# Optimization experiments

Measured on AMD Instinct MI355X. Metric: run time of the kernel, lower is better.

Reference implementation:

```python
import jax, jax.numpy as jnp
import numpy as np

NUM_HEADS = 12


def setup_inputs() -> dict:
    key = jax.random.key(0)
    ks = jax.random.split(key, 12)
    B, S, H = 8, 1024, 768
    h = jax.random.normal(ks[0], (B, S, H), dtype=jnp.float32)
    att_bias = jax.random.normal(ks[1], (B, S, S, NUM_HEADS), dtype=jnp.float32)
    mask = jax.random.randint(ks[2], (B, S, S), 0, 2, dtype=jnp.int32)
    sc = 1.0 / np.sqrt(H)
    Wq = jax.random.normal(ks[3], (H, H), dtype=jnp.float32) * sc
    bq = jax.random.normal(ks[4], (H,), dtype=jnp.float32) * 0.01
    Wk = jax.random.normal(ks[5], (H, H), dtype=jnp.float32) * sc
    bk = jax.random.normal(ks[6], (H,), dtype=jnp.float32) * 0.01
    Wv = jax.random.normal(ks[7], (H, H), dtype=jnp.float32) * sc
    bv = jax.random.normal(ks[8], (H,), dtype=jnp.float32) * 0.01
    Wo = jax.random.normal(ks[9], (H, H), dtype=jnp.float32) * sc
    bo = jax.random.normal(ks[10], (H,), dtype=jnp.float32) * 0.01
    return {"h": h, "att_bias": att_bias, "mask": mask,
            "Wq": Wq, "bq": bq, "Wk": Wk, "bk": bk,
            "Wv": Wv, "bv": bv, "Wo": Wo, "bo": bo}


def reference(h, att_bias, mask, Wq, bq, Wk, bk, Wv, bv, Wo, bo):
    B, S, H = h.shape
    nh = NUM_HEADS
    d = H // nh
    scale = d ** -0.5
    # projections -> [B, nh, S, d]
    q = (h @ Wq + bq).reshape(B, S, nh, d).transpose(0, 2, 1, 3)
    k = (h @ Wk + bk).reshape(B, S, nh, d).transpose(0, 2, 1, 3)
    v = (h @ Wv + bv).reshape(B, S, nh, d).transpose(0, 2, 1, 3)
    # scores [B, nh, S, S] + additive bias (permuted from [B,S,S,nh])
    scores = jnp.einsum('bhqd,bhkd->bhqk', q, k) * scale
    scores = scores + att_bias.transpose(0, 3, 1, 2)
    # masked_fill with 1e-14 (faithful to original: near-zero score, not -inf)
    scores = jnp.where(mask[:, None, :, :].astype(bool),
                       jnp.asarray(1e-14, scores.dtype), scores)
    attn = jax.nn.softmax(scores, axis=-1)  # dropout p=0 -> identity
    out = jnp.einsum('bhqk,bhkd->bhqd', attn, v)
    out = out.transpose(0, 2, 1, 3).reshape(B, S, H)
    return out @ Wo + bo
```

## Files before the change

kernel.cpp:

```cpp
#include <hip/hip_runtime.h>


typedef __attribute__((ext_vector_type(8))) __bf16 bf16x8;
typedef __attribute__((ext_vector_type(4))) float floatx4;
using bf16 = __bf16;

#define HID 768
#define NHEAD 12
#define DHEAD 64
#define SEQ 1024
#define NBATCH 8
#define WELEM (HID * HID)
#define QKVELEM (NBATCH * NHEAD * SEQ * DHEAD)

__device__ __forceinline__ floatx4 mfma_bf16(bf16x8 a, bf16x8 b, floatx4 c) {
  return __builtin_amdgcn_mfma_f32_16x16x32_bf16(a, b, c, 0, 0, 0);
}

#define ASYNC16(gp, lp)                                           \
  __builtin_amdgcn_global_load_lds(                               \
      (__attribute__((address_space(1))) void*)(gp),              \
      (__attribute__((address_space(3))) void*)(lp), 16, 0, 0)

__global__ void prep_weights(const float* __restrict__ Wq, const float* __restrict__ Wk,
                             const float* __restrict__ Wv, const float* __restrict__ Wo,
                             bf16* __restrict__ WT) {
  __shared__ float t[32][33];
  const int m = blockIdx.z;
  const float* W = (m == 0) ? Wq : (m == 1) ? Wk : (m == 2) ? Wv : Wo;
  const int k0 = blockIdx.x * 32, n0 = blockIdx.y * 32;
  const int tx = threadIdx.x, ty = threadIdx.y;
#pragma unroll
  for (int i = 0; i < 4; ++i)
    t[ty + 8 * i][tx] = W[(size_t)(k0 + ty + 8 * i) * HID + n0 + tx];
  __syncthreads();
  bf16* o = WT + (size_t)m * WELEM;
#pragma unroll
  for (int i = 0; i < 4; ++i)
    o[(size_t)(n0 + ty + 8 * i) * HID + k0 + tx] = (bf16)t[tx][ty + 8 * i];
}

__global__ void prep_h(const float* __restrict__ X, bf16* __restrict__ Y) {
  const size_t i = ((size_t)blockIdx.x * 256 + threadIdx.x) * 8;
  float4 a = *(const float4*)(X + i);
  float4 b = *(const float4*)(X + i + 4);
  bf16x8 o;
  o[0] = (bf16)a.x; o[1] = (bf16)a.y; o[2] = (bf16)a.z; o[3] = (bf16)a.w;
  o[4] = (bf16)b.x; o[5] = (bf16)b.y; o[6] = (bf16)b.z; o[7] = (bf16)b.w;
  *(bf16x8*)(Y + i) = o;
}

__launch_bounds__(256, 2)
__global__ void qkv_gemm(const bf16* __restrict__ A, const bf16* __restrict__ WT,
                         const float* __restrict__ bq, const float* __restrict__ bk,
                         const float* __restrict__ bv,
                         bf16* __restrict__ Qb, bf16* __restrict__ Kb,
                         bf16* __restrict__ Vb) {
  __shared__ __align__(16) bf16 As[128][32];
  __shared__ __align__(16) bf16 Bs[128][32];
  const int mat = blockIdx.z;
  const int bn = blockIdx.x * 128, bm = blockIdx.y * 128;
  const bf16* W = WT + (size_t)mat * WELEM;
  const int tid = threadIdx.x, lane = tid & 63, warp = tid >> 6;
  const int fr = lane & 15, quad = lane >> 4;
  const int wr = warp >> 1, wc = warp & 1;

  floatx4 acc[4][4] = {};

  const int srow = tid >> 2, scol = (tid & 3) * 8;
  const bf16* as0 = A + (size_t)(bm + srow) * HID + scol;
  const bf16* as1 = A + (size_t)(bm + 64 + srow) * HID + scol;
  const bf16* bs0 = W + (size_t)(bn + srow) * HID + scol;
  const bf16* bs1 = W + (size_t)(bn + 64 + srow) * HID + scol;
  bf16* la0 = &As[srow][scol];
  bf16* la1 = &As[64 + srow][scol];
  bf16* lb0 = &Bs[srow][scol];
  bf16* lb1 = &Bs[64 + srow][scol];

  for (int k0 = 0; k0 < HID; k0 += 32) {
    ASYNC16(as0 + k0, la0);
    ASYNC16(as1 + k0, la1);
    ASYNC16(bs0 + k0, lb0);
    ASYNC16(bs1 + k0, lb1);
    __syncthreads();
    bf16x8 a[4], b[4];
#pragma unroll
    for (int mi = 0; mi < 4; ++mi) a[mi] = *(const bf16x8*)&As[wr * 64 + mi * 16 + fr][quad * 8];
#pragma unroll
    for (int ni = 0; ni < 4; ++ni) b[ni] = *(const bf16x8*)&Bs[wc * 64 + ni * 16 + fr][quad * 8];
#pragma unroll
    for (int mi = 0; mi < 4; ++mi)
#pragma unroll
      for (int ni = 0; ni < 4; ++ni) acc[mi][ni] = mfma_bf16(a[mi], b[ni], acc[mi][ni]);
    __syncthreads();
  }

  const float* bias = (mat == 0) ? bq : (mat == 1) ? bk : bv;
#pragma unroll
  for (int mi = 0; mi < 4; ++mi)
#pragma unroll
    for (int ni = 0; ni < 4; ++ni)
#pragma unroll
      for (int r = 0; r < 4; ++r) {
        const int grow = bm + wr * 64 + mi * 16 + quad * 4 + r;
        const int gcol = bn + wc * 64 + ni * 16 + fr;
        float v = acc[mi][ni][r] + bias[gcol];
        const int bb = grow >> 10, ss = grow & 1023;
        const int head = gcol >> 6, dc = gcol & 63;
        const size_t bh = (size_t)bb * NHEAD + head;
        const size_t idx = (bh * SEQ + ss) * DHEAD + dc;
        if (mat == 0) Qb[idx] = (bf16)(v * 0.125f);
        else if (mat == 1) Kb[idx] = (bf16)v;
        else Vb[idx] = (bf16)v;
      }
}

__global__ void vtrans(const bf16* __restrict__ Vb, bf16* __restrict__ Vt) {
  __shared__ bf16 t[64][72];
  const int st = blockIdx.x, bh = blockIdx.y;
  const int tid = threadIdx.x;
  const bf16* src = Vb + ((size_t)bh * SEQ + st * 64) * DHEAD;
#pragma unroll
  for (int p = 0; p < 2; ++p) {
    const int r = p * 32 + (tid >> 3), c = (tid & 7) * 8;
    *(bf16x8*)&t[r][c] = *(const bf16x8*)(src + (size_t)r * DHEAD + c);
  }
  __syncthreads();
#pragma unroll
  for (int p = 0; p < 2; ++p) {
    const int d = p * 32 + (tid >> 3), s0 = (tid & 7) * 8;
    bf16x8 o;
#pragma unroll
    for (int k = 0; k < 8; ++k) o[k] = t[s0 + k][d];
    *(bf16x8*)(Vt + ((size_t)bh * DHEAD + d) * SEQ + st * 64 + s0) = o;
  }
}

__launch_bounds__(256, 2)
__global__ void attn_kernel(const bf16* __restrict__ Qb, const bf16* __restrict__ Kb,
                            const bf16* __restrict__ Vt, const float* __restrict__ bias,
                            const int* __restrict__ maskp, bf16* __restrict__ Ob) {
  __shared__ __align__(16) float Bb[2][16 * 32 * 12];
  __shared__ __align__(16) float Sc[NHEAD][16][36];

  const int qt = blockIdx.x, b = blockIdx.y;
  const int tid = threadIdx.x, lane = tid & 63, warp = tid >> 6;
  const int fr = lane & 15, quad = lane >> 4;
  const size_t brow = (size_t)b * SEQ + qt * 16;

  bf16x8 qa0[3], qa1[3];
#pragma unroll
  for (int j = 0; j < 3; ++j) {
    const size_t bh = (size_t)b * NHEAD + 3 * warp + j;
    const bf16* Qp = Qb + (bh * SEQ + qt * 16) * DHEAD;
    qa0[j] = *(const bf16x8*)(Qp + fr * DHEAD + quad * 8);
    qa1[j] = *(const bf16x8*)(Qp + fr * DHEAD + 32 + quad * 8);
  }

  float mrun[3] = {-1e30f, -1e30f, -1e30f};
  float lrun[3] = {0.f, 0.f, 0.f};
  floatx4 oacc[3][4] = {};

  const float4* biasf4 = (const float4*)bias;

  int mreg[8];
  {
#pragma unroll
    for (int i = 0; i < 6; ++i) {
      const int f = tid + 256 * i, q = f / 96, rem = f % 96;
      ASYNC16(biasf4 + ((brow + q) * SEQ + 0) * 3 + rem, (float4*)Bb[0] + f);
    }
#pragma unroll
    for (int ct = 0; ct < 2; ++ct)
#pragma unroll
      for (int r = 0; r < 4; ++r)
        mreg[ct * 4 + r] = maskp[(brow + quad * 4 + r) * SEQ + ct * 16 + fr];
  }
  __syncthreads();

  for (int ch = 0; ch < 32; ++ch) {
    const int c0 = ch * 32;
    const float* Bc = Bb[ch & 1];

    int mnext[8];
    if (ch < 31) {
      const int cn = c0 + 32;
      float* Bn = Bb[(ch + 1) & 1];
#pragma unroll
      for (int i = 0; i < 6; ++i) {
        const int f = tid + 256 * i, q = f / 96, rem = f % 96;
        ASYNC16(biasf4 + ((brow + q) * SEQ + cn) * 3 + rem, (float4*)Bn + f);
      }
#pragma unroll
      for (int ct = 0; ct < 2; ++ct)
#pragma unroll
        for (int r = 0; r < 4; ++r)
          mnext[ct * 4 + r] = maskp[(brow + quad * 4 + r) * SEQ + cn + ct * 16 + fr];
    }

#pragma unroll
    for (int ct = 0; ct < 2; ++ct) {
#pragma unroll
      for (int j = 0; j < 3; ++j) {
        const int hh = 3 * warp + j;
        const size_t bh = (size_t)b * NHEAD + hh;
        const bf16* kp = Kb + (bh * SEQ + c0 + ct * 16 + fr) * DHEAD;
        bf16x8 kb0 = *(const bf16x8*)(kp + quad * 8);
        bf16x8 kb1 = *(const bf16x8*)(kp + 32 + quad * 8);
        floatx4 st = {0.f, 0.f, 0.f, 0.f};
        st = mfma_bf16(qa0[j], kb0, st);
        st = mfma_bf16(qa1[j], kb1, st);
#pragma unroll
        for (int r = 0; r < 4; ++r) {
          const float bvl = Bc[((quad * 4 + r) * 32 + ct * 16 + fr) * 12 + hh];
          Sc[hh][quad * 4 + r][ct * 16 + fr] = mreg[ct * 4 + r] ? 0.0f : (st[r] + bvl);
        }
      }
    }

#pragma unroll
    for (int j = 0; j < 3; ++j) {
      const int hh = 3 * warp + j;
      float4 sa = *(const float4*)&Sc[hh][fr][quad * 8];
      float4 sb = *(const float4*)&Sc[hh][fr][quad * 8 + 4];
      float s[8] = {sa.x, sa.y, sa.z, sa.w, sb.x, sb.y, sb.z, sb.w};
      float mx = mrun[j];
#pragma unroll
      for (int k = 0; k < 8; ++k) mx = fmaxf(mx, s[k]);
      mx = fmaxf(mx, __shfl_xor(mx, 16));
      mx = fmaxf(mx, __shfl_xor(mx, 32));
      const float alpha = __expf(mrun[j] - mx);
      float e[8], sum = 0.f;
#pragma unroll
      for (int k = 0; k < 8; ++k) { e[k] = __expf(s[k] - mx); sum += e[k]; }
      sum += __shfl_xor(sum, 16);
      sum += __shfl_xor(sum, 32);
      lrun[j] = lrun[j] * alpha + sum;
      mrun[j] = mx;
      bf16x8 pa;
#pragma unroll
      for (int k = 0; k < 8; ++k) pa[k] = (bf16)e[k];
      float ar[4];
#pragma unroll
      for (int r = 0; r < 4; ++r) ar[r] = __shfl(alpha, quad * 4 + r);
      const size_t bh = (size_t)b * NHEAD + hh;
#pragma unroll
      for (int dvt = 0; dvt < 4; ++dvt) {
#pragma unroll
        for (int r = 0; r < 4; ++r) oacc[j][dvt][r] *= ar[r];
        const bf16* vp = Vt + (bh * DHEAD + dvt * 16 + fr) * SEQ + c0 + quad * 8;
        bf16x8 vb = *(const bf16x8*)vp;
        oacc[j][dvt] = mfma_bf16(pa, vb, oacc[j][dvt]);
      }
    }

    __syncthreads();
    if (ch < 31) {
#pragma unroll
      for (int i = 0; i < 8; ++i) mreg[i] = mnext[i];
    }
  }

#pragma unroll
  for (int j = 0; j < 3; ++j) {
    const int hh = 3 * warp + j;
    const float linv = 1.0f / lrun[j];
    float lr[4];
#pragma unroll
    for (int r = 0; r < 4; ++r) lr[r] = __shfl(linv, quad * 4 + r);
#pragma unroll
    for (int dvt = 0; dvt < 4; ++dvt)
#pragma unroll
      for (int r = 0; r < 4; ++r)
        Ob[(brow + quad * 4 + r) * HID + hh * 64 + dvt * 16 + fr] =
            (bf16)(oacc[j][dvt][r] * lr[r]);
  }
}

__launch_bounds__(256, 2)
__global__ void out_gemm(const bf16* __restrict__ A, const bf16* __restrict__ W,
                         const float* __restrict__ bo, float* __restrict__ out) {
  __shared__ __align__(16) bf16 As[128][32];
  __shared__ __align__(16) bf16 Bs[128][32];
  const int bn = blockIdx.x * 128, bm = blockIdx.y * 128;
  const int tid = threadIdx.x, lane = tid & 63, warp = tid >> 6;
  const int fr = lane & 15, quad = lane >> 4;
  const int wr = warp >> 1, wc = warp & 1;

  floatx4 acc[4][4] = {};

  const int srow = tid >> 2, scol = (tid & 3) * 8;
  const bf16* as0 = A + (size_t)(bm + srow) * HID + scol;
  const bf16* as1 = A + (size_t)(bm + 64 + srow) * HID + scol;
  const bf16* bs0 = W + (size_t)(bn + srow) * HID + scol;
  const bf16* bs1 = W + (size_t)(bn + 64 + srow) * HID + scol;
  bf16* la0 = &As[srow][scol];
  bf16* la1 = &As[64 + srow][scol];
  bf16* lb0 = &Bs[srow][scol];
  bf16* lb1 = &Bs[64 + srow][scol];

  for (int k0 = 0; k0 < HID; k0 += 32) {
    ASYNC16(as0 + k0, la0);
    ASYNC16(as1 + k0, la1);
    ASYNC16(bs0 + k0, lb0);
    ASYNC16(bs1 + k0, lb1);
    __syncthreads();
    bf16x8 a[4], b[4];
#pragma unroll
    for (int mi = 0; mi < 4; ++mi) a[mi] = *(const bf16x8*)&As[wr * 64 + mi * 16 + fr][quad * 8];
#pragma unroll
    for (int ni = 0; ni < 4; ++ni) b[ni] = *(const bf16x8*)&Bs[wc * 64 + ni * 16 + fr][quad * 8];
#pragma unroll
    for (int mi = 0; mi < 4; ++mi)
#pragma unroll
      for (int ni = 0; ni < 4; ++ni) acc[mi][ni] = mfma_bf16(a[mi], b[ni], acc[mi][ni]);
    __syncthreads();
  }

#pragma unroll
  for (int mi = 0; mi < 4; ++mi)
#pragma unroll
    for (int ni = 0; ni < 4; ++ni)
#pragma unroll
      for (int r = 0; r < 4; ++r) {
        const int grow = bm + wr * 64 + mi * 16 + quad * 4 + r;
        const int gcol = bn + wc * 64 + ni * 16 + fr;
        out[(size_t)grow * HID + gcol] = acc[mi][ni][r] + bo[gcol];
      }
}

extern "C" void kernel_launch(void* const* d_in, const int* in_sizes, int n_in,
                              void* d_out, int out_size, void* d_ws, size_t ws_size,
                              hipStream_t stream) {
  const float* h  = (const float*)d_in[0];
  const float* ab = (const float*)d_in[1];
  const int*   mk = (const int*)d_in[2];
  const float* Wq = (const float*)d_in[3];
  const float* bq = (const float*)d_in[4];
  const float* Wk = (const float*)d_in[5];
  const float* bk = (const float*)d_in[6];
  const float* Wv = (const float*)d_in[7];
  const float* bv = (const float*)d_in[8];
  const float* Wo = (const float*)d_in[9];
  const float* bo = (const float*)d_in[10];
  float* out = (float*)d_out;

  bf16* WT = (bf16*)d_ws;
  bf16* hb = WT + (size_t)4 * WELEM;
  bf16* Qb = hb + (size_t)QKVELEM;
  bf16* Kb = Qb + (size_t)QKVELEM;
  bf16* Vb = Kb + (size_t)QKVELEM;
  bf16* Vt = Vb + (size_t)QKVELEM;
  bf16* Ob = Vb;

  prep_weights<<<dim3(24, 24, 4), dim3(32, 8), 0, stream>>>(Wq, Wk, Wv, Wo, WT);
  prep_h<<<3072, 256, 0, stream>>>(h, hb);
  qkv_gemm<<<dim3(6, 64, 3), 256, 0, stream>>>(hb, WT, bq, bk, bv, Qb, Kb, Vb);
  vtrans<<<dim3(16, 96), 256, 0, stream>>>(Vb, Vt);
  attn_kernel<<<dim3(64, 8), 256, 0, stream>>>(Qb, Kb, Vt, ab, mk, Ob);
  out_gemm<<<dim3(6, 64), 256, 0, stream>>>(Ob, WT + (size_t)3 * WELEM, bo, out);
}
```

Baseline: 796.1 us.

## Split attention over two key halves with merge kernel and register-resident scores

Splits the attention kernel along the key dimension into two halves (grid z=2), each writing fp32 partial outputs and running max/sum, then merges them in a new kmerge kernel. The score tile is computed transposed so softmax stays in registers, removing the shared-memory score buffer, and the PV product now uses 16x16x16 MFMA. Bias and mask are loaded through XOR-swizzled shared buffers (single-buffered now), and launch bounds are raised to 4 blocks per CU. The aim is more blocks for occupancy on the 512-block grid and less LDS traffic, at the cost of fp32 partial writes, an extra kernel and losing the double-buffered prefetch.

Result: slower. 980.9 us (+23.2%).

```diff
diff --git a/kernel.cpp b/kernel.cpp
--- a/kernel.cpp
+++ b/kernel.cpp
@@ -2,7 +2,9 @@
 
 
 typedef __attribute__((ext_vector_type(8))) __bf16 bf16x8;
+typedef __attribute__((ext_vector_type(4))) __bf16 bf16x4;
 typedef __attribute__((ext_vector_type(4))) float floatx4;
+typedef __attribute__((ext_vector_type(4))) short short4v;
 using bf16 = __bf16;
 
 #define HID 768
@@ -12,9 +14,23 @@
 #define NBATCH 8
 #define WELEM (HID * HID)
 #define QKVELEM (NBATCH * NHEAD * SEQ * DHEAD)
+#define OPELEM QKVELEM
+#define MLROWS (NBATCH * NHEAD * SEQ)
 
 __device__ __forceinline__ floatx4 mfma_bf16(bf16x8 a, bf16x8 b, floatx4 c) {
   return __builtin_amdgcn_mfma_f32_16x16x32_bf16(a, b, c, 0, 0, 0);
+}
+
+__device__ __forceinline__ floatx4 mfma16_bf16(bf16x4 a, bf16x4 b, floatx4 c) {
+#if __has_builtin(__builtin_amdgcn_mfma_f32_16x16x16bf16_1k)
+  return __builtin_amdgcn_mfma_f32_16x16x16bf16_1k(
+      __builtin_bit_cast(short4v, a), __builtin_bit_cast(short4v, b), c, 0, 0, 0);
+#else
+  floatx4 d = c;
+  asm volatile("s_nop 1\n\tv_mfma_f32_16x16x16_bf16 %0, %1, %2, %0\n\ts_nop 4"
+               : "+v"(d) : "v"(a), "v"(b));
+  return d;
+#endif
 }
 
 #define ASYNC16(gp, lp)                                           \
@@ -136,17 +152,21 @@
   }
 }
 
-__launch_bounds__(256, 2)
+__launch_bounds__(256, 4)
 __global__ void attn_kernel(const bf16* __restrict__ Qb, const bf16* __restrict__ Kb,
                             const bf16* __restrict__ Vt, const float* __restrict__ bias,
-                            const int* __restrict__ maskp, bf16* __restrict__ Ob) {
-  __shared__ __align__(16) float Bb[2][16 * 32 * 12];
-  __shared__ __align__(16) float Sc[NHEAD][16][36];
-
-  const int qt = blockIdx.x, b = blockIdx.y;
+                            const int* __restrict__ maskp,
+                            float* __restrict__ Op, float2* __restrict__ Ml) {
+  __shared__ __align__(16) float4 BbU[1536];
+  __shared__ __align__(16) int4  MbU[128];
+
+  const int qt = blockIdx.x, b = blockIdx.y, ks = blockIdx.z;
   const int tid = threadIdx.x, lane = tid & 63, warp = tid >> 6;
   const int fr = lane & 15, quad = lane >> 4;
   const size_t brow = (size_t)b * SEQ + qt * 16;
+
+  float* Opk = Op + (size_t)ks * OPELEM;
+  float2* Mlk = Ml + (size_t)ks * MLROWS;
 
   bf16x8 qa0[3], qa1[3];
 #pragma unroll
@@ -157,124 +177,142 @@
     qa1[j] = *(const bf16x8*)(Qp + fr * DHEAD + 32 + quad * 8);
   }
 
+  const float4* bias4 = (const float4*)bias;
+  const float4* bsrc[6];
+#pragma unroll
+  for (int i = 0; i < 6; ++i) {
+    const int f = tid + 256 * i, q = f / 96, rl = f % 96;
+    const int rg = (rl & ~7) | ((rl ^ q) & 7);
+    bsrc[i] = bias4 + ((size_t)(brow + q) * SEQ) * 3 + rg;
+  }
+  const int4* msrc = nullptr;
+  if (tid < 128) {
+    const int q = tid >> 3, s = tid & 7;
+    msrc = (const int4*)(maskp + (size_t)(brow + q) * SEQ) + (s ^ (q & 7));
+  }
+
   float mrun[3] = {-1e30f, -1e30f, -1e30f};
   float lrun[3] = {0.f, 0.f, 0.f};
-  floatx4 oacc[3][4] = {};
-
-  const float4* biasf4 = (const float4*)bias;
-
-  int mreg[8];
-  {
-#pragma unroll
-    for (int i = 0; i < 6; ++i) {
-      const int f = tid + 256 * i, q = f / 96, rem = f % 96;
-      ASYNC16(biasf4 + ((brow + q) * SEQ + 0) * 3 + rem, (float4*)Bb[0] + f);
+  floatx4 oaccT[3][4] = {};
+
+  for (int ch = 0; ch < 16; ++ch) {
+    const int c0 = (ks * 16 + ch) * 32;
+
+#pragma unroll
+    for (int i = 0; i < 6; ++i) ASYNC16(bsrc[i] + c0 * 3, BbU + tid + 256 * i);
+    if (tid < 128) ASYNC16(msrc + c0 / 4, MbU + tid);
+    __syncthreads();
+
+    floatx4 st[3][2];
+#pragma unroll
+    for (int j = 0; j < 3; ++j) {
+      const size_t bh = (size_t)b * NHEAD + 3 * warp + j;
+#pragma unroll
+      for (int ct = 0; ct < 2; ++ct) {
+        const bf16* kp = Kb + (bh * SEQ + c0 + ct * 16 + fr) * DHEAD;
+        bf16x8 k0 = *(const bf16x8*)(kp + quad * 8);
+        bf16x8 k1 = *(const bf16x8*)(kp + 32 + quad * 8);
+        floatx4 t = {0.f, 0.f, 0.f, 0.f};
+        t = mfma_bf16(k0, qa0[j], t);
+        t = mfma_bf16(k1, qa1[j], t);
+        st[j][ct] = t;
+      }
     }
-#pragma unroll
-    for (int ct = 0; ct < 2; ++ct)
-#pragma unroll
-      for (int r = 0; r < 4; ++r)
-        mreg[ct * 4 + r] = maskp[(brow + quad * 4 + r) * SEQ + ct * 16 + fr];
-  }
-  __syncthreads();
-
-  for (int ch = 0; ch < 32; ++ch) {
-    const int c0 = ch * 32;
-    const float* Bc = Bb[ch & 1];
-
-    int mnext[8];
-    if (ch < 31) {
-      const int cn = c0 + 32;
-      float* Bn = Bb[(ch + 1) & 1];
-#pragma unroll
-      for (int i = 0; i < 6; ++i) {
-        const int f = tid + 256 * i, q = f / 96, rem = f % 96;
-        ASYNC16(biasf4 + ((brow + q) * SEQ + cn) * 3 + rem, (float4*)Bn + f);
-      }
-#pragma unroll
-      for (int ct = 0; ct < 2; ++ct)
-#pragma unroll
-        for (int r = 0; r < 4; ++r)
-          mnext[ct * 4 + r] = maskp[(brow + quad * 4 + r) * SEQ + cn + ct * 16 + fr];
-    }
-
+
+    const float* Bf = (const float*)BbU;
 #pragma unroll
     for (int ct = 0; ct < 2; ++ct) {
-#pragma unroll
-      for (int j = 0; j < 3; ++j) {
-        const int hh = 3 * warp + j;
-        const size_t bh = (size_t)b * NHEAD + hh;
-        const bf16* kp = Kb + (bh * SEQ + c0 + ct * 16 + fr) * DHEAD;
-        bf16x8 kb0 = *(const bf16x8*)(kp + quad * 8);
-        bf16x8 kb1 = *(const bf16x8*)(kp + 32 + quad * 8);
-        floatx4 st = {0.f, 0.f, 0.f, 0.f};
-        st = mfma_bf16(qa0[j], kb0, st);
-        st = mfma_bf16(qa1[j], kb1, st);
-#pragma unroll
-        for (int r = 0; r < 4; ++r) {
-          const float bvl = Bc[((quad * 4 + r) * 32 + ct * 16 + fr) * 12 + hh];
-          Sc[hh][quad * 4 + r][ct * 16 + fr] = mreg[ct * 4 + r] ? 0.0f : (st[r] + bvl);
+      const int4 m4 = MbU[fr * 8 + ((ct * 4 + quad) ^ (fr & 7))];
+      const int mm[4] = {m4.x, m4.y, m4.z, m4.w};
+#pragma unroll
+      for (int r = 0; r < 4; ++r) {
+        const int ug = 3 * (ct * 16 + quad * 4 + r);
+        const int u0 = fr * 96 + ((ug & ~7) | ((ug ^ fr) & 7));
+        const int u1 = fr * 96 + (((ug + 1) & ~7) | (((ug + 1) ^ fr) & 7));
+        const int u2 = fr * 96 + (((ug + 2) & ~7) | (((ug + 2) ^ fr) & 7));
+        float b0, b1, b2;
+        if (warp == 0)      { const float* p = Bf + 4 * u0; b0 = p[0]; b1 = p[1]; b2 = p[2]; }
+        else if (warp == 1) { const float* p = Bf + 4 * u1; b0 = Bf[4 * u0 + 3]; b1 = p[0]; b2 = p[1]; }
+        else if (warp == 2) { const float* p = Bf + 4 * u1; b0 = p[2]; b1 = p[3]; b2 = Bf[4 * u2]; }
+        else                { const float* p = Bf + 4 * u2; b0 = p[1]; b1 = p[2]; b2 = p[3]; }
+        if (mm[r]) {
+          st[0][ct][r] = 0.f; st[1][ct][r] = 0.f; st[2][ct][r] = 0.f;
+        } else {
+          st[0][ct][r] += b0; st[1][ct][r] += b1; st[2][ct][r] += b2;
         }
       }
     }
 
 #pragma unroll
     for (int j = 0; j < 3; ++j) {
-      const int hh = 3 * warp + j;
-      float4 sa = *(const float4*)&Sc[hh][fr][quad * 8];
-      float4 sb = *(const float4*)&Sc[hh][fr][quad * 8 + 4];
-      float s[8] = {sa.x, sa.y, sa.z, sa.w, sb.x, sb.y, sb.z, sb.w};
+      float s8[8];
+#pragma unroll
+      for (int ct = 0; ct < 2; ++ct)
+#pragma unroll
+        for (int r = 0; r < 4; ++r) s8[ct * 4 + r] = st[j][ct][r];
       float mx = mrun[j];
 #pragma unroll
-      for (int k = 0; k < 8; ++k) mx = fmaxf(mx, s[k]);
+      for (int k = 0; k < 8; ++k) mx = fmaxf(mx, s8[k]);
       mx = fmaxf(mx, __shfl_xor(mx, 16));
       mx = fmaxf(mx, __shfl_xor(mx, 32));
       const float alpha = __expf(mrun[j] - mx);
       float e[8], sum = 0.f;
 #pragma unroll
-      for (int k = 0; k < 8; ++k) { e[k] = __expf(s[k] - mx); sum += e[k]; }
+      for (int k = 0; k < 8; ++k) { e[k] = __expf(s8[k] - mx); sum += e[k]; }
       sum += __shfl_xor(sum, 16);
       sum += __shfl_xor(sum, 32);
       lrun[j] = lrun[j] * alpha + sum;
       mrun[j] = mx;
-      bf16x8 pa;
-#pragma unroll
-      for (int k = 0; k < 8; ++k) pa[k] = (bf16)e[k];
-      float ar[4];
-#pragma unroll
-      for (int r = 0; r < 4; ++r) ar[r] = __shfl(alpha, quad * 4 + r);
-      const size_t bh = (size_t)b * NHEAD + hh;
+      bf16x4 pa0, pa1;
+#pragma unroll
+      for (int r = 0; r < 4; ++r) { pa0[r] = (bf16)e[r]; pa1[r] = (bf16)e[4 + r]; }
+#pragma unroll
+      for (int dvt = 0; dvt < 4; ++dvt)
+#pragma unroll
+        for (int r = 0; r < 4; ++r) oaccT[j][dvt][r] *= alpha;
+      const size_t bh = (size_t)b * NHEAD + 3 * warp + j;
 #pragma unroll
       for (int dvt = 0; dvt < 4; ++dvt) {
-#pragma unroll
-        for (int r = 0; r < 4; ++r) oacc[j][dvt][r] *= ar[r];
-        const bf16* vp = Vt + (bh * DHEAD + dvt * 16 + fr) * SEQ + c0 + quad * 8;
-        bf16x8 vb = *(const bf16x8*)vp;
-        oacc[j][dvt] = mfma_bf16(pa, vb, oacc[j][dvt]);
+        const bf16* vp = Vt + (bh * DHEAD + dvt * 16 + fr) * SEQ + c0 + quad * 4;
+        bf16x4 v0 = *(const bf16x4*)vp;
+        bf16x4 v1 = *(const bf16x4*)(vp + 16);
+        oaccT[j][dvt] = mfma16_bf16(v0, pa0, oaccT[j][dvt]);
+        oaccT[j][dvt] = mfma16_bf16(v1, pa1, oaccT[j][dvt]);
       }
     }
 
     __syncthreads();
-    if (ch < 31) {
-#pragma unroll
-      for (int i = 0; i < 8; ++i) mreg[i] = mnext[i];
-    }
   }
 
 #pragma unroll
   for (int j = 0; j < 3; ++j) {
     const int hh = 3 * warp + j;
-    const float linv = 1.0f / lrun[j];
-    float lr[4];
-#pragma unroll
-    for (int r = 0; r < 4; ++r) lr[r] = __shfl(linv, quad * 4 + r);
+    const size_t row = ((size_t)b * NHEAD + hh) * SEQ + qt * 16 + fr;
 #pragma unroll
     for (int dvt = 0; dvt < 4; ++dvt)
-#pragma unroll
-      for (int r = 0; r < 4; ++r)
-        Ob[(brow + quad * 4 + r) * HID + hh * 64 + dvt * 16 + fr] =
-            (bf16)(oacc[j][dvt][r] * lr[r]);
-  }
+      *(floatx4*)(Opk + row * DHEAD + dvt * 16 + quad * 4) = oaccT[j][dvt];
+    if (quad == 0) Mlk[row] = make_float2(mrun[j], lrun[j]);
+  }
+}
+
+__global__ void kmerge(const float* __restrict__ O0, const float* __restrict__ O1,
+                       const float2* __restrict__ ml0, const float2* __restrict__ ml1,
+                       bf16* __restrict__ Ob) {
+  const int t = blockIdx.x * 256 + threadIdx.x;
+  const int row = t >> 4;
+  const int dq = (t & 15) * 4;
+  const float2 a = ml0[row], c = ml1[row];
+  const float M = fmaxf(a.x, c.x);
+  const float w0 = __expf(a.x - M), w1 = __expf(c.x - M);
+  const float inv = 1.0f / (a.y * w0 + c.y * w1);
+  floatx4 o0 = *(const floatx4*)(O0 + (size_t)row * DHEAD + dq);
+  floatx4 o1 = *(const floatx4*)(O1 + (size_t)row * DHEAD + dq);
+  const int bh = row >> 10, s = row & 1023;
+  const int bb = bh / NHEAD, hh = bh % NHEAD;
+  bf16x4 o;
+#pragma unroll
+  for (int r = 0; r < 4; ++r) o[r] = (bf16)((o0[r] * w0 + o1[r] * w1) * inv);
+  *(bf16x4*)(Ob + ((size_t)bb * SEQ + s) * HID + hh * DHEAD + dq) = o;
 }
 
 __launch_bounds__(256, 2)
@@ -352,11 +390,14 @@
   bf16* Vb = Kb + (size_t)QKVELEM;
   bf16* Vt = Vb + (size_t)QKVELEM;
   bf16* Ob = Vb;
+  float* Opw = (float*)(Vt + (size_t)QKVELEM);
+  float2* Mlw = (float2*)(Opw + (size_t)2 * OPELEM);
 
   prep_weights<<<dim3(24, 24, 4), dim3(32, 8), 0, stream>>>(Wq, Wk, Wv, Wo, WT);
   prep_h<<<3072, 256, 0, stream>>>(h, hb);
   qkv_gemm<<<dim3(6, 64, 3), 256, 0, stream>>>(hb, WT, bq, bk, bv, Qb, Kb, Vb);
   vtrans<<<dim3(16, 96), 256, 0, stream>>>(Vb, Vt);
-  attn_kernel<<<dim3(64, 8), 256, 0, stream>>>(Qb, Kb, Vt, ab, mk, Ob);
+  attn_kernel<<<dim3(64, 8, 2), 256, 0, stream>>>(Qb, Kb, Vt, ab, mk, Opw, Mlw);
+  kmerge<<<6144, 256, 0, stream>>>(Opw, Opw + OPELEM, Mlw, Mlw + MLROWS, Ob);
   out_gemm<<<dim3(6, 64), 256, 0, stream>>>(Ob, WT + (size_t)3 * WELEM, bo, out);
 }
```
